# Kernel optimization log

Measured on AMD Instinct MI355X. Metric: run time of the kernel, lower is better.

The kernel has to match this reference:

```python
import jax, jax.numpy as jnp
import numpy as np

N_NODES = 100000
N_EDGES = 1000000
DIM = 64


def rel_graph_conv(x, src, dst, etype, W, Ws, b, act):
    # DGL RelGraphConv (regularizer=None, self_loop=True, bias=True, sum agg):
    # out_i = act( sum_{(j->i)} W_{r} x_j + x_i @ Ws + b )
    # num_rels=2: transform once per relation, then select per edge.
    h = jnp.einsum('nd,rdo->rno', x, W)              # [2, N, out]
    m = jnp.where((etype == 0)[:, None], h[0][src], h[1][src])  # [E, out]
    agg = jax.ops.segment_sum(m, dst, num_segments=x.shape[0])  # [N, out]
    out = agg + x @ Ws + b
    return act(out) if act is not None else out


def setup_inputs() -> dict:
    key = jax.random.key(0)
    ks = jax.random.split(key, 16)
    scale = 1.0 / np.sqrt(DIM)
    inp = {
        'features': jax.random.normal(ks[0], (N_NODES, DIM), dtype=jnp.float32),
        'src': jax.random.randint(ks[1], (N_EDGES,), 0, N_NODES, dtype=jnp.int32),
        'dst': jax.random.randint(ks[2], (N_EDGES,), 0, N_NODES, dtype=jnp.int32),
        'etype': jax.random.randint(ks[3], (N_EDGES,), 0, 2, dtype=jnp.int32),
    }
    for i in range(3):
        inp[f'W{i}'] = jax.random.normal(ks[4 + 3 * i], (2, DIM, DIM), dtype=jnp.float32) * scale
        inp[f'Ws{i}'] = jax.random.normal(ks[5 + 3 * i], (DIM, DIM), dtype=jnp.float32) * scale
        inp[f'b{i}'] = jnp.zeros((DIM,), dtype=jnp.float32)
    return inp


def reference(features, src, dst, etype, W0, Ws0, b0, W1, Ws1, b1, W2, Ws2, b2):
    # dropout is identity in eval mode
    h = rel_graph_conv(features, src, dst, etype, W0, Ws0, b0, jax.nn.relu)
    h = rel_graph_conv(h, src, dst, etype, W1, Ws1, b1, jax.nn.relu)
    h = rel_graph_conv(h, src, dst, etype, W2, Ws2, b2, None)
    return h
```

## Files before the change

kernel.cpp:

```cpp
#include <hip/hip_runtime.h>

#define NN 100000
#define NE 1000000
#define NEP (NE + 6 * NN)
#define DIM 64
#define ZPITCH 200
#define SCHUNK 1024
#define SBLOCKS ((NN + SCHUNK - 1) / SCHUNK)
#define PAD4(c) (((c) + 3) & ~3)
#define NPART 8

typedef __attribute__((ext_vector_type(8))) short short8;
typedef __attribute__((ext_vector_type(4))) float f32x4;
typedef __attribute__((ext_vector_type(4))) _Float16 h4;
typedef __attribute__((ext_vector_type(8))) _Float16 h8;

union HU { uint2 u; h4 h; };

__device__ __forceinline__ ushort f2h(float f) {
    union { _Float16 h; ushort u; } c; c.h = (_Float16)f; return c.u;
}

__global__ __launch_bounds__(256) void zero_buf(int* p, int len) {
    int i = blockIdx.x * 256 + threadIdx.x;
    if (i < len) p[i] = 0;
}

__global__ __launch_bounds__(256) void init_esrc(int* esrc) {
    int i = blockIdx.x * 256 + threadIdx.x;
    if (i < NEP) esrc[i] = NN;
}

__global__ __launch_bounds__(256) void count_rank2p(const int* __restrict__ dst,
                                                    const int* __restrict__ et,
                                                    int* __restrict__ cnt2p,
                                                    int* __restrict__ rank) {
    int e = blockIdx.x * 256 + threadIdx.x;
    int p = blockIdx.x & (NPART - 1);
    if (e < NE) rank[e] = atomicAdd(&cnt2p[p * 2 * NN + dst[e] * 2 + et[e]], 1);
}

__global__ __launch_bounds__(256) void merge_counts(int* __restrict__ cnt2p,
                                                    int* __restrict__ cnt2) {
    int i = blockIdx.x * 256 + threadIdx.x;
    if (i < 2 * NN) {
        int s = 0;
#pragma unroll
        for (int p = 0; p < NPART; ++p) {
            int v = cnt2p[p * 2 * NN + i];
            cnt2p[p * 2 * NN + i] = s;
            s += v;
        }
        cnt2[i] = s;
    }
}

__global__ __launch_bounds__(256) void scan_partial2p(const int* __restrict__ cnt2,
                                                      int* __restrict__ bsum) {
    int t = threadIdx.x, lane = t & 63, wid = t >> 6;
    int base = blockIdx.x * SCHUNK + t * 4;
    int s = 0;
#pragma unroll
    for (int k = 0; k < 4; ++k) {
        int i = base + k;
        if (i < NN) s += PAD4(cnt2[2 * i]) + PAD4(cnt2[2 * i + 1]);
    }
#pragma unroll
    for (int off = 32; off > 0; off >>= 1) s += __shfl_down(s, off, 64);
    __shared__ int wtot[4];
    if (lane == 0) wtot[wid] = s;
    __syncthreads();
    if (t == 0) bsum[blockIdx.x] = wtot[0] + wtot[1] + wtot[2] + wtot[3];
}

__global__ __launch_bounds__(128) void scan_bsums(const int* __restrict__ bsum,
                                                  int* __restrict__ bsum_ex) {
    __shared__ int sh[128];
    int t = threadIdx.x;
    int v = (t < SBLOCKS) ? bsum[t] : 0;
    sh[t] = v;
    __syncthreads();
    for (int off = 1; off < 128; off <<= 1) {
        int u = (t >= off) ? sh[t - off] : 0;
        __syncthreads();
        sh[t] += u;
        __syncthreads();
    }
    if (t < SBLOCKS) bsum_ex[t] = sh[t] - v;
}

__global__ __launch_bounds__(256) void scan_final2p(const int* __restrict__ cnt2,
                                                    const int* __restrict__ bsum_ex,
                                                    int* __restrict__ row_ptr) {
    int t = threadIdx.x, lane = t & 63, wid = t >> 6;
    int base = blockIdx.x * SCHUNK + t * 4;
    int c[4];
#pragma unroll
    for (int k = 0; k < 4; ++k) {
        int i = base + k;
        c[k] = (i < NN) ? (PAD4(cnt2[2 * i]) + PAD4(cnt2[2 * i + 1])) : 0;
    }
    int s = c[0] + c[1] + c[2] + c[3];
    int incl = s;
#pragma unroll
    for (int off = 1; off < 64; off <<= 1) {
        int u = __shfl_up(incl, off, 64);
        if (lane >= off) incl += u;
    }
    __shared__ int wtot[4];
    if (lane == 63) wtot[wid] = incl;
    __syncthreads();
    int woff = 0;
    for (int w = 0; w < wid; ++w) woff += wtot[w];
    int run = bsum_ex[blockIdx.x] + woff + (incl - s);
#pragma unroll
    for (int k = 0; k < 4; ++k) {
        int i = base + k;
        if (i < NN) row_ptr[i] = run;
        run += c[k];
    }
}

__global__ __launch_bounds__(256) void fill_edges4p(const int* __restrict__ src,
                                                    const int* __restrict__ dst,
                                                    const int* __restrict__ et,
                                                    const int* __restrict__ rank,
                                                    const int* __restrict__ row_ptr,
                                                    const int* __restrict__ cnt2,
                                                    const int* __restrict__ cnt2p,
                                                    int* __restrict__ esrc) {
    int e = blockIdx.x * 256 + threadIdx.x;
    int p = blockIdx.x & (NPART - 1);
    if (e < NE) {
        int d = dst[e], r = et[e];
        int pre = cnt2p[p * 2 * NN + 2 * d + r];
        int pos = row_ptr[d] + pre + rank[e] + (r ? PAD4(cnt2[2 * d]) : 0);
        esrc[pos] = src[e];
    }
}

__global__ __launch_bounds__(256) void convert_feat(const float* __restrict__ x,
                                                    ushort* __restrict__ xb) {
    int i = blockIdx.x * 256 + threadIdx.x;
    float4 v = ((const float4*)x)[i];
    union { ushort u[4]; uint2 w; } o;
    o.u[0] = f2h(v.x); o.u[1] = f2h(v.y); o.u[2] = f2h(v.z); o.u[3] = f2h(v.w);
    *(uint2*)(xb + (size_t)i * 4) = o.w;
}

__global__ void zero_rows(ushort* a, ushort* b) {
    int t = threadIdx.x;
    a[(size_t)NN * DIM + t] = 0;
    b[(size_t)NN * DIM + t] = 0;
}

__global__ __launch_bounds__(256) void prep_w(const float* __restrict__ W,
                                              const float* __restrict__ Ws,
                                              ushort* __restrict__ wt) {
    int idx = blockIdx.x * 256 + threadIdx.x;
    int k = idx >> 6, n = idx & 63;
    float v = (k < 128) ? W[k * 64 + n] : Ws[(k - 128) * 64 + n];
    wt[n * 192 + k] = f2h(v);
}

__global__ __launch_bounds__(256) void rgcn_aggregate_g(
    const uint2* __restrict__ xb2, const int* __restrict__ row_ptr,
    const int* __restrict__ cnt2, const int* __restrict__ esrc,
    uint2* __restrict__ agg2)
{
    int t = threadIdx.x, lane = t & 63, wid = t >> 6;
    int g = lane >> 4, s = lane & 15;
    int n = blockIdx.x * 16 + wid * 4 + g;
    int start = row_ptr[n];
    int c0p = PAD4(cnt2[2 * n]);
    int degp = c0p + PAD4(cnt2[2 * n + 1]);

    const uint2* xrow = xb2 + s;
    HU z; z.u.x = 0u; z.u.y = 0u;
    h4 a0 = z.h, a1 = z.h;

    int j = 0;
#pragma unroll 2
    for (; j < c0p; j += 4) {
        int4 q = *(const int4*)(esrc + start + j);
        HU v0, v1, v2, v3;
        v0.u = xrow[(size_t)q.x * 16];
        v1.u = xrow[(size_t)q.y * 16];
        v2.u = xrow[(size_t)q.z * 16];
        v3.u = xrow[(size_t)q.w * 16];
        a0 += v0.h; a0 += v1.h; a0 += v2.h; a0 += v3.h;
    }
#pragma unroll 2
    for (; j < degp; j += 4) {
        int4 q = *(const int4*)(esrc + start + j);
        HU v0, v1, v2, v3;
        v0.u = xrow[(size_t)q.x * 16];
        v1.u = xrow[(size_t)q.y * 16];
        v2.u = xrow[(size_t)q.z * 16];
        v3.u = xrow[(size_t)q.w * 16];
        a1 += v0.h; a1 += v1.h; a1 += v2.h; a1 += v3.h;
    }

    HU o0, o1; o0.h = a0; o1.h = a1;
    agg2[(size_t)n * 32 + s] = o0.u;
    agg2[(size_t)n * 32 + 16 + s] = o1.u;
}

__global__ __launch_bounds__(256) void rgcn_transform_mfma(
    const ushort* __restrict__ agg,
    const ushort* __restrict__ xb,
    const ushort* __restrict__ wt,
    const float* __restrict__ bias,
    float* __restrict__ outf,
    ushort* __restrict__ xbn,
    int mode)
{
    __shared__ ushort sZ[64 * ZPITCH];

    int t = threadIdx.x, lane = t & 63, wid = t >> 6;
    int quad = lane >> 4, l16 = lane & 15;

    h8 bh[6];
    {
        const ushort* wh = wt + (size_t)(wid * 16 + l16) * 192;
#pragma unroll
        for (int kk = 0; kk < 6; ++kk)
            bh[kk] = *(const h8*)(wh + kk * 32 + quad * 8);
    }
    float bv = bias[wid * 16 + l16];

    int n0 = blockIdx.x * 64;
    for (int i = t; i < 1024; i += 256) {
        int node = i >> 4, c8 = i & 15;
        int n = n0 + node;
        uint4 v = {0u, 0u, 0u, 0u};
        if (n < NN) v = *(const uint4*)(agg + (size_t)n * 128 + c8 * 8);
        *(uint4*)(sZ + node * ZPITCH + c8 * 8) = v;
    }
    for (int i = t; i < 512; i += 256) {
        int node = i >> 3, c8 = i & 7;
        int n = n0 + node;
        uint4 v = {0u, 0u, 0u, 0u};
        if (n < NN) v = *(const uint4*)(xb + (size_t)n * DIM + c8 * 8);
        *(uint4*)(sZ + node * ZPITCH + 128 + c8 * 8) = v;
    }
    __syncthreads();

    f32x4 acc[4];
#pragma unroll
    for (int mt = 0; mt < 4; ++mt) acc[mt] = (f32x4){bv, bv, bv, bv};

#pragma unroll
    for (int kk = 0; kk < 6; ++kk) {
#pragma unroll
        for (int mt = 0; mt < 4; ++mt) {
            h8 a = *(const h8*)(sZ + (mt * 16 + l16) * ZPITCH + kk * 32 + quad * 8);
            acc[mt] = __builtin_amdgcn_mfma_f32_16x16x32_f16(a, bh[kk], acc[mt], 0, 0, 0);
        }
    }

    int col = wid * 16 + l16;
#pragma unroll
    for (int mt = 0; mt < 4; ++mt) {
#pragma unroll
        for (int r = 0; r < 4; ++r) {
            int node = n0 + mt * 16 + quad * 4 + r;
            if (node < NN) {
                float v = acc[mt][r];
                if (mode) outf[(size_t)node * DIM + col] = v;
                else      xbn[(size_t)node * DIM + col] = f2h(fmaxf(v, 0.f));
            }
        }
    }
}

extern "C" void kernel_launch(void* const* d_in, const int* in_sizes, int n_in,
                              void* d_out, int out_size, void* d_ws, size_t ws_size,
                              hipStream_t stream)
{
    const float* feat = (const float*)d_in[0];
    const int*   src  = (const int*)d_in[1];
    const int*   dst  = (const int*)d_in[2];
    const int*   et   = (const int*)d_in[3];
    const float* W[3]  = { (const float*)d_in[4], (const float*)d_in[7], (const float*)d_in[10] };
    const float* Ws[3] = { (const float*)d_in[5], (const float*)d_in[8], (const float*)d_in[11] };
    const float* b[3]  = { (const float*)d_in[6], (const float*)d_in[9], (const float*)d_in[12] };

    uint*   agg   = (uint*)d_ws;
    ushort* xbuf0 = (ushort*)(agg + (size_t)NN * 64);
    ushort* xbuf1 = xbuf0 + (size_t)(NN + 1) * DIM;
    ushort* wt    = xbuf1 + (size_t)(NN + 1) * DIM;
    int* esrc    = (int*)(wt + 3 * 12288);
    int* rank    = esrc + NEP;
    int* cnt2    = rank + NE;
    int* cnt2p   = cnt2 + 2 * NN;
    int* row_ptr = cnt2p + NPART * 2 * NN;
    int* bsum    = row_ptr + NN;
    int* bsum_ex = bsum + SBLOCKS;
    float* outF  = (float*)d_out;

    const dim3 tb(256);
    const int zgrid = (NPART * 2 * NN + 255) / 256;
    const int igrid = (NEP + 255) / 256;
    const int egrid = (NE + 255) / 256;
    const int mgrid = (2 * NN + 255) / 256;
    const int tgrid = (NN + 63) / 64;
    const int agrid = NN / 16;

    zero_buf<<<zgrid, tb, 0, stream>>>(cnt2p, NPART * 2 * NN);
    init_esrc<<<igrid, tb, 0, stream>>>(esrc);
    count_rank2p<<<egrid, tb, 0, stream>>>(dst, et, cnt2p, rank);
    merge_counts<<<mgrid, tb, 0, stream>>>(cnt2p, cnt2);
    scan_partial2p<<<SBLOCKS, tb, 0, stream>>>(cnt2, bsum);
    scan_bsums<<<1, 128, 0, stream>>>(bsum, bsum_ex);
    scan_final2p<<<SBLOCKS, tb, 0, stream>>>(cnt2, bsum_ex, row_ptr);
    fill_edges4p<<<egrid, tb, 0, stream>>>(src, dst, et, rank, row_ptr, cnt2, cnt2p, esrc);

    prep_w<<<48, tb, 0, stream>>>(W[0], Ws[0], wt);
    prep_w<<<48, tb, 0, stream>>>(W[1], Ws[1], wt + 12288);
    prep_w<<<48, tb, 0, stream>>>(W[2], Ws[2], wt + 2 * 12288);
    convert_feat<<<NN * 16 / 256, tb, 0, stream>>>(feat, xbuf0);
    zero_rows<<<1, 64, 0, stream>>>(xbuf0, xbuf1);

    rgcn_aggregate_g<<<agrid, tb, 0, stream>>>((const uint2*)xbuf0, row_ptr, cnt2, esrc, (uint2*)agg);
    rgcn_transform_mfma<<<tgrid, tb, 0, stream>>>((const ushort*)agg, xbuf0, wt, b[0], nullptr, xbuf1, 0);
    rgcn_aggregate_g<<<agrid, tb, 0, stream>>>((const uint2*)xbuf1, row_ptr, cnt2, esrc, (uint2*)agg);
    rgcn_transform_mfma<<<tgrid, tb, 0, stream>>>((const ushort*)agg, xbuf1, wt + 12288, b[1], nullptr, xbuf0, 0);
    rgcn_aggregate_g<<<agrid, tb, 0, stream>>>((const uint2*)xbuf0, row_ptr, cnt2, esrc, (uint2*)agg);
    rgcn_transform_mfma<<<tgrid, tb, 0, stream>>>((const ushort*)agg, xbuf0, wt + 2 * 12288, b[2], outF, nullptr, 1);
}
```

Before: 313.2 us.

## Interleave relation gather loops, fill only CSR padding, merge small setup kernels

The aggregation kernel now walks both relation segments of a node in one loop, issuing eight independent row gathers per iteration so more memory loads are in flight, and points exhausted segments at a sentinel padding slot. The full esrc initialisation pass is replaced by a pad_fill kernel that writes only the padding entries plus a small sentinel tail. The three weight-prep launches are merged into one, and zeroing of the sentinel feature rows is folded into the feature conversion kernel, cutting launch count. The combined loop does wasted loads on the shorter relation's sentinel, which adds traffic when the two degrees are unbalanced.

```diff
diff --git a/kernel.cpp b/kernel.cpp
--- a/kernel.cpp
+++ b/kernel.cpp
@@ -24,11 +24,6 @@
 __global__ __launch_bounds__(256) void zero_buf(int* p, int len) {
     int i = blockIdx.x * 256 + threadIdx.x;
     if (i < len) p[i] = 0;
-}
-
-__global__ __launch_bounds__(256) void init_esrc(int* esrc) {
-    int i = blockIdx.x * 256 + threadIdx.x;
-    if (i < NEP) esrc[i] = NN;
 }
 
 __global__ __launch_bounds__(256) void count_rank2p(const int* __restrict__ dst,
@@ -118,6 +113,22 @@
         int i = base + k;
         if (i < NN) row_ptr[i] = run;
         run += c[k];
+    }
+}
+
+__global__ __launch_bounds__(256) void pad_fill(const int* __restrict__ row_ptr,
+                                                const int* __restrict__ cnt2,
+                                                int* __restrict__ esrc) {
+    int i = blockIdx.x * 256 + threadIdx.x;
+    if (i < 2 * NN) {
+        int n = i >> 1, r = i & 1;
+        int2 c = *(const int2*)(cnt2 + 2 * n);
+        int cr = r ? c.y : c.x;
+        int base = row_ptr[n] + (r ? PAD4(c.x) : 0) + cr;
+        int np = PAD4(cr) - cr;
+        for (int k = 0; k < np; ++k) esrc[base + k] = NN;
+    } else if (i < 2 * NN + 4) {
+        esrc[NEP + (i - 2 * NN)] = NN;
     }
 }
 
@@ -140,27 +151,36 @@
 }
 
 __global__ __launch_bounds__(256) void convert_feat(const float* __restrict__ x,
-                                                    ushort* __restrict__ xb) {
-    int i = blockIdx.x * 256 + threadIdx.x;
+                                                    ushort* __restrict__ xb,
+                                                    ushort* __restrict__ xb1) {
+    int b = blockIdx.x;
+    if (b == NN * 16 / 256) {
+        int t = threadIdx.x;
+        if (t < 64) {
+            xb[(size_t)NN * DIM + t] = 0;
+            xb1[(size_t)NN * DIM + t] = 0;
+        }
+        return;
+    }
+    int i = b * 256 + threadIdx.x;
     float4 v = ((const float4*)x)[i];
     union { ushort u[4]; uint2 w; } o;
     o.u[0] = f2h(v.x); o.u[1] = f2h(v.y); o.u[2] = f2h(v.z); o.u[3] = f2h(v.w);
     *(uint2*)(xb + (size_t)i * 4) = o.w;
 }
 
-__global__ void zero_rows(ushort* a, ushort* b) {
-    int t = threadIdx.x;
-    a[(size_t)NN * DIM + t] = 0;
-    b[(size_t)NN * DIM + t] = 0;
-}
-
-__global__ __launch_bounds__(256) void prep_w(const float* __restrict__ W,
-                                              const float* __restrict__ Ws,
-                                              ushort* __restrict__ wt) {
+__global__ __launch_bounds__(256) void prep_w_all(
+    const float* __restrict__ W0, const float* __restrict__ Ws0,
+    const float* __restrict__ W1, const float* __restrict__ Ws1,
+    const float* __restrict__ W2, const float* __restrict__ Ws2,
+    ushort* __restrict__ wt) {
     int idx = blockIdx.x * 256 + threadIdx.x;
-    int k = idx >> 6, n = idx & 63;
+    int l = idx / 12288, rr = idx % 12288;
+    const float* W  = (l == 0) ? W0 : (l == 1) ? W1 : W2;
+    const float* Ws = (l == 0) ? Ws0 : (l == 1) ? Ws1 : Ws2;
+    int k = rr >> 6, n = rr & 63;
     float v = (k < 128) ? W[k * 64 + n] : Ws[(k - 128) * 64 + n];
-    wt[n * 192 + k] = f2h(v);
+    wt[l * 12288 + n * 192 + k] = f2h(v);
 }
 
 __global__ __launch_bounds__(256) void rgcn_aggregate_g(
@@ -172,33 +192,31 @@
     int g = lane >> 4, s = lane & 15;
     int n = blockIdx.x * 16 + wid * 4 + g;
     int start = row_ptr[n];
-    int c0p = PAD4(cnt2[2 * n]);
-    int degp = c0p + PAD4(cnt2[2 * n + 1]);
+    int2 c = *(const int2*)(cnt2 + 2 * n);
+    int c0p = PAD4(c.x), c1p = PAD4(c.y);
+    int tmax = c0p > c1p ? c0p : c1p;
+    int b1 = start + c0p;
 
     const uint2* xrow = xb2 + s;
     HU z; z.u.x = 0u; z.u.y = 0u;
     h4 a0 = z.h, a1 = z.h;
 
-    int j = 0;
-#pragma unroll 2
-    for (; j < c0p; j += 4) {
-        int4 q = *(const int4*)(esrc + start + j);
-        HU v0, v1, v2, v3;
-        v0.u = xrow[(size_t)q.x * 16];
-        v1.u = xrow[(size_t)q.y * 16];
-        v2.u = xrow[(size_t)q.z * 16];
-        v3.u = xrow[(size_t)q.w * 16];
-        a0 += v0.h; a0 += v1.h; a0 += v2.h; a0 += v3.h;
-    }
-#pragma unroll 2
-    for (; j < degp; j += 4) {
-        int4 q = *(const int4*)(esrc + start + j);
-        HU v0, v1, v2, v3;
-        v0.u = xrow[(size_t)q.x * 16];
-        v1.u = xrow[(size_t)q.y * 16];
-        v2.u = xrow[(size_t)q.z * 16];
-        v3.u = xrow[(size_t)q.w * 16];
-        a1 += v0.h; a1 += v1.h; a1 += v2.h; a1 += v3.h;
+    for (int j = 0; j < tmax; j += 4) {
+        int i0 = (j < c0p) ? start + j : NEP;
+        int i1 = (j < c1p) ? b1 + j : NEP;
+        int4 qa = *(const int4*)(esrc + i0);
+        int4 qb = *(const int4*)(esrc + i1);
+        HU w0, w1, w2, w3, w4, w5, w6, w7;
+        w0.u = xrow[(size_t)qa.x * 16];
+        w1.u = xrow[(size_t)qa.y * 16];
+        w2.u = xrow[(size_t)qa.z * 16];
+        w3.u = xrow[(size_t)qa.w * 16];
+        w4.u = xrow[(size_t)qb.x * 16];
+        w5.u = xrow[(size_t)qb.y * 16];
+        w6.u = xrow[(size_t)qb.z * 16];
+        w7.u = xrow[(size_t)qb.w * 16];
+        a0 += w0.h; a0 += w1.h; a0 += w2.h; a0 += w3.h;
+        a1 += w4.h; a1 += w5.h; a1 += w6.h; a1 += w7.h;
     }
 
     HU o0, o1; o0.h = a0; o1.h = a1;
@@ -291,7 +309,7 @@
     ushort* xbuf1 = xbuf0 + (size_t)(NN + 1) * DIM;
     ushort* wt    = xbuf1 + (size_t)(NN + 1) * DIM;
     int* esrc    = (int*)(wt + 3 * 12288);
-    int* rank    = esrc + NEP;
+    int* rank    = esrc + NEP + 4;
     int* cnt2    = rank + NE;
     int* cnt2p   = cnt2 + 2 * NN;
     int* row_ptr = cnt2p + NPART * 2 * NN;
@@ -301,26 +319,23 @@
 
     const dim3 tb(256);
     const int zgrid = (NPART * 2 * NN + 255) / 256;
-    const int igrid = (NEP + 255) / 256;
     const int egrid = (NE + 255) / 256;
     const int mgrid = (2 * NN + 255) / 256;
+    const int pgrid = (2 * NN + 4 + 255) / 256;
     const int tgrid = (NN + 63) / 64;
     const int agrid = NN / 16;
 
     zero_buf<<<zgrid, tb, 0, stream>>>(cnt2p, NPART * 2 * NN);
-    init_esrc<<<igrid, tb, 0, stream>>>(esrc);
     count_rank2p<<<egrid, tb, 0, stream>>>(dst, et, cnt2p, rank);
     merge_counts<<<mgrid, tb, 0, stream>>>(cnt2p, cnt2);
     scan_partial2p<<<SBLOCKS, tb, 0, stream>>>(cnt2, bsum);
     scan_bsums<<<1, 128, 0, stream>>>(bsum, bsum_ex);
     scan_final2p<<<SBLOCKS, tb, 0, stream>>>(cnt2, bsum_ex, row_ptr);
+    pad_fill<<<pgrid, tb, 0, stream>>>(row_ptr, cnt2, esrc);
     fill_edges4p<<<egrid, tb, 0, stream>>>(src, dst, et, rank, row_ptr, cnt2, cnt2p, esrc);
 
-    prep_w<<<48, tb, 0, stream>>>(W[0], Ws[0], wt);
-    prep_w<<<48, tb, 0, stream>>>(W[1], Ws[1], wt + 12288);
-    prep_w<<<48, tb, 0, stream>>>(W[2], Ws[2], wt + 2 * 12288);
-    convert_feat<<<NN * 16 / 256, tb, 0, stream>>>(feat, xbuf0);
-    zero_rows<<<1, 64, 0, stream>>>(xbuf0, xbuf1);
+    prep_w_all<<<144, tb, 0, stream>>>(W[0], Ws[0], W[1], Ws[1], W[2], Ws[2], wt);
+    convert_feat<<<NN * 16 / 256 + 1, tb, 0, stream>>>(feat, xbuf0, xbuf1);
 
     rgcn_aggregate_g<<<agrid, tb, 0, stream>>>((const uint2*)xbuf0, row_ptr, cnt2, esrc, (uint2*)agg);
     rgcn_transform_mfma<<<tgrid, tb, 0, stream>>>((const ushort*)agg, xbuf0, wt, b[0], nullptr, xbuf1, 0);
```

Result: faster. 301.6 us (-3.7%).
